# Optimization experiments

Hardware: AMD Instinct MI355X
Metric: run time of the kernel (lower is better)

## Reference

```python
import jax, jax.numpy as jnp
import numpy as np

B, N, M, C = 2, 8192, 1024, 1152  # batch, dense points, centers, feature dim
K = 3                              # three_nn interpolation
EPS = 1e-8


def setup_inputs() -> dict:
    key = jax.random.key(0)
    k1, k2, k3 = jax.random.split(key, 3)
    xyz = jax.random.normal(k1, (B, N, 3), dtype=jnp.float32)      # query points
    center = jax.random.normal(k2, (B, M, 3), dtype=jnp.float32)   # center coords (already permuted to B,M,3)
    feats = jax.random.normal(k3, (B, C, M), dtype=jnp.float32)    # backbone features at centers
    return {"xyz": xyz, "center": center, "feats": feats}


def _interpolate(xyz, center, feats):
    # Squared pairwise distances [B, N, M] (PointNet++ three_nn uses squared dists).
    d2 = (jnp.sum(xyz * xyz, axis=-1, keepdims=True)
          + jnp.sum(center * center, axis=-1)[:, None, :]
          - 2.0 * jnp.einsum('bnd,bmd->bnm', xyz, center))
    neg_top, idx = jax.lax.top_k(-d2, K)          # 3 nearest centers per point
    dist = -neg_top                                # [B, N, K] squared distances
    recip = 1.0 / (dist + EPS)
    weight = recip / jnp.sum(recip, axis=-1, keepdims=True)  # [B, N, K]
    fm = jnp.transpose(feats, (0, 2, 1))           # [B, M, C]
    batch_idx = jnp.arange(B)[:, None, None]       # broadcast gather over batch
    gathered = fm[batch_idx, idx]                  # [B, N, K, C]
    out = jnp.einsum('bnkc,bnk->bcn', gathered, weight)  # [B, C, N]
    return out


def reference(xyz, center, feats):
    return _interpolate(xyz, center, feats)
```

## Files before the change

kernel.cpp:

```cpp
#include <hip/hip_runtime.h>
#include <cstdint>

#define B_ 2
#define N_ 8192
#define M_ 1024
#define C_ 1152
#define EPS_ 1e-8f
#define NT 32
#define CHUNK 128

__device__ __forceinline__ unsigned short f2bf(float f) {
    unsigned u = __float_as_uint(f);
    u += 0x7fffu + ((u >> 16) & 1u);
    return (unsigned short)(u >> 16);
}
__device__ __forceinline__ float bf2f(unsigned short h) {
    return __uint_as_float(((unsigned)h) << 16);
}

__global__ __launch_bounds__(256) void k_transpose(const float* __restrict__ feats,
                                                   unsigned short* __restrict__ fm) {
    __shared__ float tile[64][65];
    int m0 = blockIdx.x * 64;
    int c0 = blockIdx.y * 64;
    int b  = blockIdx.z;
    int tx = threadIdx.x;
    int ty = threadIdx.y;
    const float* src = feats + ((size_t)b * C_ + c0) * M_ + m0;
#pragma unroll
    for (int j = 0; j < 16; ++j) {
        int cl = ty + 4 * j;
        tile[cl][tx] = __builtin_nontemporal_load(&src[(size_t)cl * M_ + tx]);
    }
    __syncthreads();
    unsigned short* dst = fm + ((size_t)b * M_ + m0) * C_ + c0;
#pragma unroll
    for (int j = 0; j < 16; ++j) {
        int ml = ty + 4 * j;
        dst[(size_t)ml * C_ + tx] = f2bf(tile[tx][ml]);
    }
}

__device__ __forceinline__ unsigned long long pack_di(float d, int m) {
    unsigned u = __float_as_uint(d);
    unsigned s = (unsigned)((int)u >> 31);
    u ^= (s | 0x80000000u);
    return ((unsigned long long)u << 32) | (unsigned)m;
}
__device__ __forceinline__ float unpack_d(unsigned long long k) {
    unsigned u = (unsigned)(k >> 32);
    unsigned s = (unsigned)((int)u >> 31);
    u ^= (~s | 0x80000000u);
    return __uint_as_float(u);
}
__device__ __forceinline__ void kinsert(unsigned long long p,
        unsigned long long& k0, unsigned long long& k1, unsigned long long& k2) {
    unsigned long long t;
    bool c0 = p < k0; t = c0 ? k0 : p; k0 = c0 ? p : k0; p = t;
    bool c1 = p < k1; t = c1 ? k1 : p; k1 = c1 ? p : k1; p = t;
    k2 = (p < k2) ? p : k2;
}
__device__ __forceinline__ unsigned long long shfl_xor_u64(unsigned long long v, int off) {
    int lo = __shfl_xor((int)(unsigned)v, off);
    int hi = __shfl_xor((int)(unsigned)(v >> 32), off);
    return ((unsigned long long)(unsigned)hi << 32) | (unsigned)lo;
}

#define NC 16
#define PTS 16

__global__ __launch_bounds__(256) void k_threenn(const float* __restrict__ xyz,
                                                 const float* __restrict__ center,
                                                 int* __restrict__ idx_ws,
                                                 float* __restrict__ w_ws) {
    __shared__ float4 sc[M_];
    int b  = blockIdx.y;
    int n0 = blockIdx.x * PTS;
    int t  = threadIdx.x;
    for (int i = t; i < M_; i += 256) {
        float cx = center[((size_t)b * M_ + i) * 3 + 0];
        float cy = center[((size_t)b * M_ + i) * 3 + 1];
        float cz = center[((size_t)b * M_ + i) * 3 + 2];
        float cc = __fadd_rn(__fadd_rn(__fmul_rn(cx, cx), __fmul_rn(cy, cy)),
                             __fmul_rn(cz, cz));
        sc[i] = make_float4(cx, cy, cz, cc);
    }
    __syncthreads();

    int p = t >> 4;
    int c = t & 15;
    int n = n0 + p;
    float x = xyz[((size_t)b * N_ + n) * 3 + 0];
    float y = xyz[((size_t)b * N_ + n) * 3 + 1];
    float z = xyz[((size_t)b * N_ + n) * 3 + 2];
    float xx = __fadd_rn(__fadd_rn(__fmul_rn(x, x), __fmul_rn(y, y)),
                         __fmul_rn(z, z));

    unsigned long long k0 = ~0ull, k1 = ~0ull, k2 = ~0ull;
#pragma unroll 4
    for (int it = 0; it < M_ / NC; ++it) {
        int m = c + it * NC;
        float4 v = sc[m];
        float dot = __fmaf_rn(z, v.z, __fmaf_rn(y, v.y, __fmul_rn(x, v.x)));
        float d   = __fsub_rn(__fadd_rn(xx, v.w), __fmul_rn(2.0f, dot));
        kinsert(pack_di(d, m), k0, k1, k2);
    }
#pragma unroll
    for (int off = 1; off <= 8; off <<= 1) {
        unsigned long long e0 = shfl_xor_u64(k0, off);
        unsigned long long e1 = shfl_xor_u64(k1, off);
        unsigned long long e2 = shfl_xor_u64(k2, off);
        kinsert(e0, k0, k1, k2);
        kinsert(e1, k0, k1, k2);
        kinsert(e2, k0, k1, k2);
    }
    if (c == 0) {
        float r0 = 1.0f / __fadd_rn(unpack_d(k0), EPS_);
        float r1 = 1.0f / __fadd_rn(unpack_d(k1), EPS_);
        float r2 = 1.0f / __fadd_rn(unpack_d(k2), EPS_);
        float s  = __fadd_rn(__fadd_rn(r0, r1), r2);
        size_t base = ((size_t)b * N_ + n) * 3;
        idx_ws[base + 0] = (int)(unsigned)k0;
        idx_ws[base + 1] = (int)(unsigned)k1;
        idx_ws[base + 2] = (int)(unsigned)k2;
        w_ws[base + 0] = r0 / s; w_ws[base + 1] = r1 / s; w_ws[base + 2] = r2 / s;
    }
}

__global__ __launch_bounds__(256) void k_interp(const unsigned short* __restrict__ fm,
                                                const int* __restrict__ idx_ws,
                                                const float* __restrict__ w_ws,
                                                float* __restrict__ out) {
    __shared__ float T[NT][CHUNK + 1];
    __shared__ int   sbase[NT][3];
    __shared__ float sw[NT][3];
    int b  = blockIdx.z;
    int c0 = blockIdx.y * CHUNK;
    int n0 = blockIdx.x * NT;
    int t  = threadIdx.x;
    if (t < NT) {
        size_t ib = ((size_t)b * N_ + n0 + t) * 3;
#pragma unroll
        for (int k = 0; k < 3; ++k) {
            sbase[t][k] = (b * M_ + idx_ws[ib + k]) * C_;
            sw[t][k]    = w_ws[ib + k];
        }
    }
    __syncthreads();
    int wave = t >> 6;
    int lane = t & 63;
#pragma unroll
    for (int pp = 0; pp < 8; ++pp) {
        int p = wave * 8 + pp;
        float w0 = sw[p][0], w1 = sw[p][1], w2 = sw[p][2];
        const ushort2 a0 = *(const ushort2*)(fm + sbase[p][0] + c0 + 2 * lane);
        const ushort2 a1 = *(const ushort2*)(fm + sbase[p][1] + c0 + 2 * lane);
        const ushort2 a2 = *(const ushort2*)(fm + sbase[p][2] + c0 + 2 * lane);
        float sx = __fmaf_rn(bf2f(a2.x), w2, __fmaf_rn(bf2f(a1.x), w1, __fmul_rn(bf2f(a0.x), w0)));
        float sy = __fmaf_rn(bf2f(a2.y), w2, __fmaf_rn(bf2f(a1.y), w1, __fmul_rn(bf2f(a0.y), w0)));
        T[p][2 * lane]     = sx;
        T[p][2 * lane + 1] = sy;
    }
    __syncthreads();
    int p   = t & 31;
    int ccb = t >> 5;
#pragma unroll
    for (int i = 0; i < 16; ++i) {
        int cc = i * 8 + ccb;
        __builtin_nontemporal_store(T[p][cc],
            &out[((size_t)b * C_ + c0 + cc) * N_ + n0 + p]);
    }
}

extern "C" void kernel_launch(void* const* d_in, const int* in_sizes, int n_in,
                              void* d_out, int out_size, void* d_ws, size_t ws_size,
                              hipStream_t stream) {
    const float* xyz    = (const float*)d_in[0];
    const float* center = (const float*)d_in[1];
    const float* feats  = (const float*)d_in[2];
    float* out = (float*)d_out;

    char*           ws     = (char*)d_ws;
    unsigned short* fm     = (unsigned short*)ws;
    int*            idx_ws = (int*)(ws + (size_t)B_ * M_ * C_ * 2);
    float*          w_ws   = (float*)(ws + (size_t)B_ * M_ * C_ * 2 + (size_t)B_ * N_ * 3 * 4);

    k_transpose<<<dim3(M_ / 64, C_ / 64, B_), dim3(64, 4), 0, stream>>>(feats, fm);
    k_threenn <<<dim3(N_ / PTS, B_), 256, 0, stream>>>(xyz, center, idx_ws, w_ws);
    k_interp  <<<dim3(N_ / NT, C_ / CHUNK, B_), 256, 0, stream>>>(fm, idx_ws, w_ws, out);
}
```

Before: 44.90 us.

## Vectorize interp gathers/stores and remap blocks so each XCD handles one batch

The interpolation kernel now gathers 4 bf16 values per lane (ushort4) instead of 2 and writes output as 16-byte float4 nontemporal stores instead of scalar stores. The grid is flattened, and block indices are remapped so that the 8 round-robin XCD slots split by batch and neighbouring tiles. The goal is better L2 locality for the fm gathers and fewer, wider memory transactions. The transposed reads from LDS during the store phase may cause bank conflicts.

After: 41.95 us. 6.6% less time.

```diff
diff --git a/kernel.cpp b/kernel.cpp
--- a/kernel.cpp
+++ b/kernel.cpp
@@ -8,6 +8,10 @@
 #define EPS_ 1e-8f
 #define NT 32
 #define CHUNK 128
+#define NBN (N_ / NT)
+#define NBC (C_ / CHUNK)
+
+typedef float f32x4 __attribute__((ext_vector_type(4)));
 
 __device__ __forceinline__ unsigned short f2bf(float f) {
     unsigned u = __float_as_uint(f);
@@ -134,10 +138,13 @@
     __shared__ float T[NT][CHUNK + 1];
     __shared__ int   sbase[NT][3];
     __shared__ float sw[NT][3];
-    int b  = blockIdx.z;
-    int c0 = blockIdx.y * CHUNK;
-    int n0 = blockIdx.x * NT;
-    int t  = threadIdx.x;
+    int flat = blockIdx.x;
+    int slot = flat & 7;
+    int b    = slot >> 2;
+    int idx  = (flat >> 3) * 4 + (slot & 3);
+    int n0   = (idx & (NBN - 1)) * NT;
+    int c0   = (idx >> 8) * CHUNK;
+    int t    = threadIdx.x;
     if (t < NT) {
         size_t ib = ((size_t)b * N_ + n0 + t) * 3;
 #pragma unroll
@@ -149,26 +156,29 @@
     __syncthreads();
     int wave = t >> 6;
     int lane = t & 63;
-#pragma unroll
-    for (int pp = 0; pp < 8; ++pp) {
-        int p = wave * 8 + pp;
+    int half = lane >> 5;
+    int cl   = (lane & 31) * 4;
+#pragma unroll
+    for (int pp = 0; pp < 4; ++pp) {
+        int p = pp * 8 + wave * 2 + half;
         float w0 = sw[p][0], w1 = sw[p][1], w2 = sw[p][2];
-        const ushort2 a0 = *(const ushort2*)(fm + sbase[p][0] + c0 + 2 * lane);
-        const ushort2 a1 = *(const ushort2*)(fm + sbase[p][1] + c0 + 2 * lane);
-        const ushort2 a2 = *(const ushort2*)(fm + sbase[p][2] + c0 + 2 * lane);
-        float sx = __fmaf_rn(bf2f(a2.x), w2, __fmaf_rn(bf2f(a1.x), w1, __fmul_rn(bf2f(a0.x), w0)));
-        float sy = __fmaf_rn(bf2f(a2.y), w2, __fmaf_rn(bf2f(a1.y), w1, __fmul_rn(bf2f(a0.y), w0)));
-        T[p][2 * lane]     = sx;
-        T[p][2 * lane + 1] = sy;
-    }
-    __syncthreads();
-    int p   = t & 31;
-    int ccb = t >> 5;
-#pragma unroll
-    for (int i = 0; i < 16; ++i) {
-        int cc = i * 8 + ccb;
-        __builtin_nontemporal_store(T[p][cc],
-            &out[((size_t)b * C_ + c0 + cc) * N_ + n0 + p]);
+        const ushort4 a0 = *(const ushort4*)(fm + sbase[p][0] + c0 + cl);
+        const ushort4 a1 = *(const ushort4*)(fm + sbase[p][1] + c0 + cl);
+        const ushort4 a2 = *(const ushort4*)(fm + sbase[p][2] + c0 + cl);
+        T[p][cl + 0] = __fmaf_rn(bf2f(a2.x), w2, __fmaf_rn(bf2f(a1.x), w1, __fmul_rn(bf2f(a0.x), w0)));
+        T[p][cl + 1] = __fmaf_rn(bf2f(a2.y), w2, __fmaf_rn(bf2f(a1.y), w1, __fmul_rn(bf2f(a0.y), w0)));
+        T[p][cl + 2] = __fmaf_rn(bf2f(a2.z), w2, __fmaf_rn(bf2f(a1.z), w1, __fmul_rn(bf2f(a0.z), w0)));
+        T[p][cl + 3] = __fmaf_rn(bf2f(a2.w), w2, __fmaf_rn(bf2f(a1.w), w1, __fmul_rn(bf2f(a0.w), w0)));
+    }
+    __syncthreads();
+    int p4  = (t & 7) * 4;
+    int ccb = t >> 3;
+#pragma unroll
+    for (int r = 0; r < 4; ++r) {
+        int cc = r * 32 + ccb;
+        f32x4 v = { T[p4 + 0][cc], T[p4 + 1][cc], T[p4 + 2][cc], T[p4 + 3][cc] };
+        __builtin_nontemporal_store(v,
+            (f32x4*)&out[((size_t)b * C_ + c0 + cc) * N_ + n0 + p4]);
     }
 }
 
@@ -187,5 +197,5 @@
 
     k_transpose<<<dim3(M_ / 64, C_ / 64, B_), dim3(64, 4), 0, stream>>>(feats, fm);
     k_threenn <<<dim3(N_ / PTS, B_), 256, 0, stream>>>(xyz, center, idx_ws, w_ws);
-    k_interp  <<<dim3(N_ / NT, C_ / CHUNK, B_), 256, 0, stream>>>(fm, idx_ws, w_ws, out);
-}
+    k_interp  <<<NBN * NBC * B_, 256, 0, stream>>>(fm, idx_ws, w_ws, out);
+}
```
